# Performance work log

Measured on AMD Instinct MI355X. Metric: run time of the kernel, lower is better.

Reference implementation:

```python
import jax, jax.numpy as jnp
import numpy as np

B, N, DIM, HEADS, DH = 2, 1024, 1024, 16, 64
SEQ_LEN, MEM_NUM = 1024, 4
EH, EW, ET = 4, 4, 1  # mem_expand_size
PH, PW = 4, 4        # patch grid
CUR_PATCH_IDX = 5
MEM_IDXS = [0, 1, 4, 5]


def _locate(idx):
    # get_pos_from_idx_down_right
    num_frame = PH * PW
    inner = idx % num_frame
    return (inner % PH, inner // PH, idx // num_frame)


def _rel_idxs():
    rph, rpw = 2 * EH + 1, 2 * EW + 1
    frame = rph * rpw
    src = _locate(CUR_PATCH_IDX)
    out = []
    for t in MEM_IDXS + [CUR_PATCH_IDX]:
        tg = _locate(t)
        out.append((tg[0] - src[0] + EH) * rpw + (tg[1] - src[1] + EW) + (tg[2] - src[2] + ET) * frame)
    return np.array(out, np.int32)


def setup_inputs() -> dict:
    key = jax.random.key(0)
    ks = jax.random.split(key, 8)
    inner = HEADS * DH
    s = 0.02
    return {
        "x": jax.random.normal(ks[0], (B, N, DIM), jnp.float32),
        "mem": jax.random.normal(ks[1], (B, MEM_NUM * SEQ_LEN, DIM), jnp.float32),
        "mask": jnp.zeros((B, MEM_NUM * SEQ_LEN + N), bool),
        "rel_idxs": jnp.asarray(_rel_idxs()),
        "Wq": jax.random.normal(ks[2], (DIM, inner), jnp.float32) * s,
        "Wk": jax.random.normal(ks[3], (DIM, inner), jnp.float32) * s,
        "Wv": jax.random.normal(ks[4], (DIM, inner), jnp.float32) * s,
        "Wo": jax.random.normal(ks[5], (inner, DIM), jnp.float32) * s,
        "bo": jnp.zeros((DIM,), jnp.float32),
        "rel_table": jax.random.normal(ks[6], ((2 * EH + 1) * (2 * EW + 1) * (2 * ET + 1), HEADS), jnp.float32) * s,
    }


def reference(x, mem, mask, rel_idxs, Wq, Wk, Wv, Wo, bo, rel_table):
    b, n, dim = x.shape
    heads = rel_table.shape[1]
    dh = Wq.shape[1] // heads
    mem_num = rel_idxs.shape[0] - 1
    mem_len = mem.shape[1]
    seq_len = mem_len // mem_num
    scale = dh ** (-0.5)

    kx = jnp.concatenate([mem, x], axis=1)           # [b, j, dim]
    j = kx.shape[1]
    q = (x @ Wq).reshape(b, n, heads, dh).transpose(0, 2, 1, 3)   # bhid
    k = (kx @ Wk).reshape(b, j, heads, dh).transpose(0, 2, 1, 3)  # bhjd
    v = (kx @ Wv).reshape(b, j, heads, dh).transpose(0, 2, 1, 3)

    # relative position bias: a per-head scalar added to every K feature
    rel_emb = rel_table[rel_idxs].T                  # [h, mem_num+1]
    bias_mem = jnp.repeat(rel_emb[:, :mem_num], seq_len, axis=1)  # [h, mem_len]
    bias_cur = jnp.broadcast_to(rel_emb[:, -1:], (heads, j - mem_len))
    bias = jnp.concatenate([bias_mem, bias_cur], axis=1)          # [h, j]
    k = k + bias[None, :, :, None]

    dots = jnp.einsum('bhid,bhjd->bhij', q, k) * scale
    neg = -jnp.finfo(dots.dtype).max
    dots = jnp.where(mask[:, None, None, :], neg, dots)
    causal = jnp.triu(jnp.ones((n, j), bool), j - n + 1)
    dots = jnp.where(causal, neg, dots)

    attn = jax.nn.softmax(dots, axis=-1)
    out = jnp.einsum('bhij,bhjd->bhid', attn, v)
    out = out.transpose(0, 2, 1, 3).reshape(b, n, heads * dh) @ Wo + bo
    new_mem = x[:, -seq_len:]
    return out, new_mem
```

## Files before the change

kernel.cpp:

```cpp
#include <hip/hip_runtime.h>
#include <float.h>

#define NQ    1024
#define JTOT  5120
#define MEML  4096
#define SCL2  0.18033688011112042f

typedef __attribute__((ext_vector_type(8))) short bf16x8;
typedef __attribute__((ext_vector_type(8))) unsigned short ush8;
typedef __attribute__((ext_vector_type(4))) unsigned short ush4;
typedef __attribute__((ext_vector_type(4))) float f32x4;

static __device__ __forceinline__ unsigned short f2bf(float x) {
    union { float f; unsigned u; } v; v.f = x;
    unsigned r = (v.u + 0x7fffu + ((v.u >> 16) & 1u)) >> 16;
    return (unsigned short)r;
}
static __device__ __forceinline__ unsigned pack2(float f0, float f1) {
    union { float f; unsigned u; } a, b; a.f = f1; b.f = f0;
    return __builtin_amdgcn_perm(a.u, b.u, 0x07060302u);
}

static __device__ __forceinline__ void gld16(const void* g, void* l) {
    __builtin_amdgcn_global_load_lds(
        (const __attribute__((address_space(1))) unsigned int*)g,
        (__attribute__((address_space(3))) unsigned int*)l, 16, 0, 0);
}

__global__ __launch_bounds__(256)
void prep_kernel(const float* __restrict__ x, const float* __restrict__ mem,
                 const unsigned char* __restrict__ mask,
                 const float* __restrict__ W0, const float* __restrict__ W1,
                 const float* __restrict__ W2, const float* __restrict__ W3,
                 unsigned short* __restrict__ xb, unsigned short* __restrict__ memb,
                 unsigned short* __restrict__ wt, float* __restrict__ mbp)
{
    __shared__ float Ts[32][33];
    const int bid = blockIdx.x;
    const int t   = threadIdx.x;
    if (bid < 5120) {
        const float* src = (bid < 1024) ? x : mem;
        unsigned short* dst = (bid < 1024) ? xb : memb;
        const size_t i = (size_t)((bid < 1024) ? bid : bid - 1024) * 2048 + t * 8;
        float4 a = *(const float4*)(src + i);
        float4 b = *(const float4*)(src + i + 4);
        ush8 o;
        o[0] = f2bf(a.x); o[1] = f2bf(a.y); o[2] = f2bf(a.z); o[3] = f2bf(a.w);
        o[4] = f2bf(b.x); o[5] = f2bf(b.y); o[6] = f2bf(b.z); o[7] = f2bf(b.w);
        *(ush8*)(dst + i) = o;
    } else if (bid < 5160) {
        const int i = (bid - 5120) * 256 + t;
        mbp[i] = mask[i] ? -1.0e30f : 0.0f;
    } else {
        const int idx = bid - 5160;
        const int z   = idx >> 10;
        const int rem = idx & 1023;
        const float* W = (z == 0) ? W0 : (z == 1) ? W1 : (z == 2) ? W2 : W3;
        unsigned short* D = wt + (size_t)z * 1024 * 1024;
        const int n0 = (rem & 31) * 32, k0 = (rem >> 5) * 32;
        const int tr = t >> 3, tc = (t & 7) * 4;
        float4 v = *(const float4*)(W + (size_t)(k0 + tr) * 1024 + n0 + tc);
        Ts[tr][tc + 0] = v.x; Ts[tr][tc + 1] = v.y;
        Ts[tr][tc + 2] = v.z; Ts[tr][tc + 3] = v.w;
        __syncthreads();
        ush4 o;
        o[0] = f2bf(Ts[tc + 0][tr]); o[1] = f2bf(Ts[tc + 1][tr]);
        o[2] = f2bf(Ts[tc + 2][tr]); o[3] = f2bf(Ts[tc + 3][tr]);
        *(ush4*)(D + (size_t)(n0 + tr) * 1024 + k0 + tc) = o;
    }
}

__global__ __launch_bounds__(256)
void mgemm01_kernel(const unsigned short* __restrict__ xb,
                    const unsigned short* __restrict__ memb,
                    const unsigned short* __restrict__ wt,
                    unsigned short* __restrict__ Qb, unsigned short* __restrict__ Kb,
                    unsigned short* __restrict__ Vb,
                    const float* __restrict__ rel_table, const int* __restrict__ rel_idxs)
{
    __shared__ unsigned short Al[128 * 64];
    __shared__ unsigned short Bl[128 * 64];

    const int t    = threadIdx.x;
    const int lane = t & 63;
    const int w    = t >> 6;
    const int wr   = w >> 1, wc = w & 1;
    const int l15  = lane & 15;
    const int quad = lane >> 4;
    const int l7   = l15 & 7;

    int bid = blockIdx.x;
    int mode, bx, by;
    if (bid < 384) { mode = 0; bx = bid % 24; by = bid / 24; }
    else           { mode = 1; bid -= 384; bx = bid & 15; by = bid >> 4; }
    const int mat = bx >> 3;
    const int n0  = (bx & 7) * 128;
    const int m0  = by * 128;
    const unsigned short* A = (mode == 0) ? xb : memb;
    const unsigned short* B = wt + (size_t)((mode == 0) ? mat : mat + 1) * 1024 * 1024;

    f32x4 acc[4][4];
    #pragma unroll
    for (int i = 0; i < 4; i++)
        #pragma unroll
        for (int j = 0; j < 4; j++) acc[i][j] = (f32x4){0.f, 0.f, 0.f, 0.f};

    for (int k0 = 0; k0 < 1024; k0 += 64) {
        __syncthreads();
        #pragma unroll
        for (int it = 0; it < 4; it++) {
            const int lin  = it * 256 + t;
            const int row  = lin >> 3;
            const int colb = ((lin & 7) ^ (row & 7)) * 8;
            unsigned short* albase = &Al[(size_t)(it * 256 + w * 64) * 8];
            unsigned short* blbase = &Bl[(size_t)(it * 256 + w * 64) * 8];
            gld16(A + (size_t)(m0 + row) * 1024 + k0 + colb, albase);
            gld16(B + (size_t)(n0 + row) * 1024 + k0 + colb, blbase);
        }
        __syncthreads();
        bf16x8 af[4][2], bfr[4][2];
        #pragma unroll
        for (int i = 0; i < 4; i++) {
            const int R = wr * 64 + i * 16 + l15;
            af[i][0] = *(const bf16x8*)&Al[R * 64 + ((quad ^ l7) << 3)];
            af[i][1] = *(const bf16x8*)&Al[R * 64 + (((4 | quad) ^ l7) << 3)];
        }
        #pragma unroll
        for (int j = 0; j < 4; j++) {
            const int R = wc * 64 + j * 16 + l15;
            bfr[j][0] = *(const bf16x8*)&Bl[R * 64 + ((quad ^ l7) << 3)];
            bfr[j][1] = *(const bf16x8*)&Bl[R * 64 + (((4 | quad) ^ l7) << 3)];
        }
        #pragma unroll
        for (int i = 0; i < 4; i++)
            #pragma unroll
            for (int j = 0; j < 4; j++) {
                acc[i][j] = __builtin_amdgcn_mfma_f32_16x16x32_bf16(af[i][0], bfr[j][0], acc[i][j], 0, 0, 0);
                acc[i][j] = __builtin_amdgcn_mfma_f32_16x16x32_bf16(af[i][1], bfr[j][1], acc[i][j], 0, 0, 0);
            }
    }

    const bool isQ = (mode == 0) && (mat == 0);
    const bool isK = (mode == 0) ? (mat == 1) : (mat == 0);
    if (!isQ && !isK) {
        #pragma unroll
        for (int i = 0; i < 4; i++) {
            const int r0 = m0 + wr * 64 + i * 16 + quad * 4;
            const int bb = (mode == 0) ? (r0 >> 10) : (r0 >> 12);
            const int j0 = (mode == 0) ? 4096 + (r0 & 1023) : (r0 & 4095);
            #pragma unroll
            for (int jb = 0; jb < 4; jb++) {
                const int col = n0 + wc * 64 + jb * 16 + l15;
                ush4 o;
                o[0] = f2bf(acc[i][jb][0]); o[1] = f2bf(acc[i][jb][1]);
                o[2] = f2bf(acc[i][jb][2]); o[3] = f2bf(acc[i][jb][3]);
                *(ush4*)(Vb + ((size_t)((bb * 16 + (col >> 6)) * 64 + (col & 63))) * JTOT + j0) = o;
            }
        }
    } else {
        #pragma unroll
        for (int i = 0; i < 4; i++)
            #pragma unroll
            for (int reg = 0; reg < 4; reg++) {
                const int r = m0 + wr * 64 + i * 16 + quad * 4 + reg;
                int bb, idx, chunk;
                if (mode == 0) { bb = r >> 10; idx = isK ? 4096 + (r & 1023) : (r & 1023); chunk = 4; }
                else           { bb = r >> 12; idx = r & 4095; chunk = idx >> 10; }
                #pragma unroll
                for (int jb = 0; jb < 4; jb++) {
                    const int col = n0 + wc * 64 + jb * 16 + l15;
                    const int hh = col >> 6, dh = col & 63;
                    float v = acc[i][jb][reg];
                    if (isK) {
                        v += rel_table[rel_idxs[chunk] * 16 + hh];
                        Kb[((size_t)(bb * 16 + hh) * JTOT + idx) * 64 + dh] = f2bf(v);
                    } else {
                        Qb[((size_t)(bb * 16 + hh) * NQ + idx) * 64 + dh] = f2bf(v);
                    }
                }
            }
    }
}

__global__ __launch_bounds__(256)
void mgemm2_kernel(const unsigned short* __restrict__ A,
                   const unsigned short* __restrict__ WT,
                   float* __restrict__ outF, const float* __restrict__ bo,
                   const float* __restrict__ x, float* __restrict__ newmem)
{
    __shared__ unsigned short Al[64 * 64];
    __shared__ unsigned short Bl[128 * 64];

    const int t = threadIdx.x;
    if (blockIdx.z == 1) {
        const int blk = blockIdx.y * 8 + blockIdx.x;
        const size_t base = (size_t)blk * 8192 + t * 4;
        #pragma unroll
        for (int i = 0; i < 8; i++)
            *(float4*)(newmem + base + (size_t)i * 1024) =
                *(const float4*)(x + base + (size_t)i * 1024);
        return;
    }

    const int lane = t & 63;
    const int w    = t >> 6;
    const int l15  = lane & 15;
    const int quad = lane >> 4;
    const int l7   = l15 & 7;
    const int n0   = blockIdx.x * 128;
    const int m0   = blockIdx.y * 64;

    f32x4 acc[4][2];
    #pragma unroll
    for (int i = 0; i < 4; i++)
        #pragma unroll
        for (int j = 0; j < 2; j++) acc[i][j] = (f32x4){0.f, 0.f, 0.f, 0.f};

    for (int k0 = 0; k0 < 1024; k0 += 64) {
        __syncthreads();
        #pragma unroll
        for (int it = 0; it < 2; it++) {
            const int lin  = it * 256 + t;
            const int row  = lin >> 3;
            const int colb = ((lin & 7) ^ (row & 7)) * 8;
            gld16(A + (size_t)(m0 + row) * 1024 + k0 + colb,
                  &Al[(size_t)(it * 256 + w * 64) * 8]);
        }
        #pragma unroll
        for (int it = 0; it < 4; it++) {
            const int lin  = it * 256 + t;
            const int row  = lin >> 3;
            const int colb = ((lin & 7) ^ (row & 7)) * 8;
            gld16(WT + (size_t)(n0 + row) * 1024 + k0 + colb,
                  &Bl[(size_t)(it * 256 + w * 64) * 8]);
        }
        __syncthreads();
        bf16x8 af[4][2], bfr[2][2];
        #pragma unroll
        for (int i = 0; i < 4; i++) {
            const int R = i * 16 + l15;
            af[i][0] = *(const bf16x8*)&Al[R * 64 + ((quad ^ l7) << 3)];
            af[i][1] = *(const bf16x8*)&Al[R * 64 + (((4 | quad) ^ l7) << 3)];
        }
        #pragma unroll
        for (int j = 0; j < 2; j++) {
            const int R = w * 32 + j * 16 + l15;
            bfr[j][0] = *(const bf16x8*)&Bl[R * 64 + ((quad ^ l7) << 3)];
            bfr[j][1] = *(const bf16x8*)&Bl[R * 64 + (((4 | quad) ^ l7) << 3)];
        }
        #pragma unroll
        for (int i = 0; i < 4; i++)
            #pragma unroll
            for (int j = 0; j < 2; j++) {
                acc[i][j] = __builtin_amdgcn_mfma_f32_16x16x32_bf16(af[i][0], bfr[j][0], acc[i][j], 0, 0, 0);
                acc[i][j] = __builtin_amdgcn_mfma_f32_16x16x32_bf16(af[i][1], bfr[j][1], acc[i][j], 0, 0, 0);
            }
    }

    #pragma unroll
    for (int i = 0; i < 4; i++)
        #pragma unroll
        for (int reg = 0; reg < 4; reg++) {
            const int r = m0 + i * 16 + quad * 4 + reg;
            #pragma unroll
            for (int j = 0; j < 2; j++) {
                const int col = n0 + w * 32 + j * 16 + l15;
                outF[(size_t)r * 1024 + col] = acc[i][j][reg] + bo[col];
            }
        }
}

__global__ __launch_bounds__(256)
void attn5_kernel(const unsigned short* __restrict__ qh,
                  const unsigned short* __restrict__ kh,
                  const unsigned short* __restrict__ vt,
                  const float* __restrict__ mb,
                  unsigned short* __restrict__ ao)
{
    __shared__ unsigned short Ks[128 * 64];
    __shared__ unsigned short Vs[64 * 128];
    __shared__ unsigned short Ps[64 * 128];

    const int t    = threadIdx.x;
    const int lane = t & 63;
    const int w    = t >> 6;
    const int l15  = lane & 15;
    const int quad = lane >> 4;
    const int l7   = l15 & 7;
    const int qt   = blockIdx.x;
    const int h    = blockIdx.y;
    const int b    = blockIdx.z;
    const int qbase = qt * 64;
    const int qg    = qbase + w * 16 + l15;

    const unsigned short* qrow = qh + (((size_t)(b * 16 + h) * NQ + qg) << 6);
    const bf16x8 bq0 = *(const bf16x8*)(qrow + quad * 8);
    const bf16x8 bq1 = *(const bf16x8*)(qrow + 32 + quad * 8);

    const int krow = t >> 3;
    const int kcol = (t & 7) * 8;
    const int ksw  = ((t & 7) ^ (krow & 7)) * 8;
    const int vrow = t >> 4;
    const int vu   = t & 15;
    const int vcol = vu * 8;
    const int vsw  = ((vu & 8) | ((vu ^ (vrow & 7)) & 7)) * 8;

    const unsigned short* kbase = kh + (((size_t)(b * 16 + h) * JTOT) << 6);
    const unsigned short* vbase = vt + (((size_t)(b * 16 + h)) << 6) * JTOT;
    const float* mbb = mb + b * JTOT;

    f32x4 oa[4];
    #pragma unroll
    for (int mt = 0; mt < 4; mt++) oa[mt] = (f32x4){0.f, 0.f, 0.f, 0.f};
    float l_i = 0.f;

    const int ntp = (qt + 66) >> 1;

    ush8 kst[4], vst[4];
    #pragma unroll
    for (int p = 0; p < 4; p++)
        kst[p] = *(const ush8*)(kbase + ((size_t)(krow + 32 * p) << 6) + kcol);
    #pragma unroll
    for (int p = 0; p < 4; p++)
        vst[p] = *(const ush8*)(vbase + (size_t)(vrow + 16 * p) * JTOT + vcol);

    for (int jt = 0; jt < ntp; jt++) {
        const int jbase = jt * 128;
        __syncthreads();
        #pragma unroll
        for (int p = 0; p < 4; p++)
            *(ush8*)&Ks[(krow + 32 * p) * 64 + ksw] = kst[p];
        #pragma unroll
        for (int p = 0; p < 4; p++)
            *(ush8*)&Vs[(vrow + 16 * p) * 128 + vsw] = vst[p];
        __syncthreads();

        if (jt + 1 < ntp) {
            const int jb2 = jbase + 128;
            #pragma unroll
            for (int p = 0; p < 4; p++)
                kst[p] = *(const ush8*)(kbase + ((size_t)(jb2 + krow + 32 * p) << 6) + kcol);
            #pragma unroll
            for (int p = 0; p < 4; p++)
                vst[p] = *(const ush8*)(vbase + (size_t)(vrow + 16 * p) * JTOT + jb2 + vcol);
        }

        f32x4 sa[8];
        #pragma unroll
        for (int mt2 = 0; mt2 < 8; mt2++) {
            const int ra = (mt2 * 16 + l15) * 64;
            const bf16x8 ak0 = *(const bf16x8*)&Ks[ra + ((quad ^ l7) << 3)];
            const bf16x8 ak1 = *(const bf16x8*)&Ks[ra + (((4 | quad) ^ l7) << 3)];
            f32x4 s = (f32x4){0.f, 0.f, 0.f, 0.f};
            s = __builtin_amdgcn_mfma_f32_16x16x32_bf16(ak0, bq0, s, 0, 0, 0);
            s = __builtin_amdgcn_mfma_f32_16x16x32_bf16(ak1, bq1, s, 0, 0, 0);
            sa[mt2] = s;
        }

        #pragma unroll
        for (int mt2 = 0; mt2 < 8; mt2++) {
            const float4 mv = *(const float4*)(mbb + jbase + mt2 * 16 + quad * 4);
            sa[mt2][0] = sa[mt2][0] * SCL2 + mv.x;
            sa[mt2][1] = sa[mt2][1] * SCL2 + mv.y;
            sa[mt2][2] = sa[mt2][2] * SCL2 + mv.z;
            sa[mt2][3] = sa[mt2][3] * SCL2 + mv.w;
        }
        if (jt == ntp - 1) {
            const int tl = qg + 4096 - jbase;
            #pragma unroll
            for (int mt2 = 0; mt2 < 8; mt2++)
                #pragma unroll
                for (int r = 0; r < 4; r++)
                    if (mt2 * 16 + quad * 4 + r > tl) sa[mt2][r] = -1.0e30f;
        }

        #pragma unroll
        for (int mt2 = 0; mt2 < 8; mt2++)
            #pragma unroll
            for (int r = 0; r < 4; r++) {
                const float pv = __builtin_amdgcn_exp2f(sa[mt2][r]);
                sa[mt2][r] = pv;
                l_i += pv;
            }

        const int prow = (w * 16 + l15) * 128;
        #pragma unroll
        for (int mt2 = 0; mt2 < 8; mt2++) {
            const int u  = 2 * mt2 + (quad >> 1);
            const int up = (u & 8) | ((u ^ l7) & 7);
            uint2 pk;
            pk.x = pack2(sa[mt2][0], sa[mt2][1]);
            pk.y = pack2(sa[mt2][2], sa[mt2][3]);
            *(uint2*)&Ps[prow + up * 8 + (quad & 1) * 4] = pk;
        }

        #pragma unroll
        for (int s = 0; s < 4; s++) {
            const int u  = quad + 4 * s;
            const int up = (u & 8) | ((u ^ l7) & 7);
            const bf16x8 bp = *(const bf16x8*)&Ps[prow + up * 8];
            #pragma unroll
            for (int mt = 0; mt < 4; mt++) {
                const bf16x8 av = *(const bf16x8*)&Vs[(mt * 16 + l15) * 128 + up * 8];
                oa[mt] = __builtin_amdgcn_mfma_f32_16x16x32_bf16(av, bp, oa[mt], 0, 0, 0);
            }
        }
    }

    float l = l_i;
    l += __shfl_xor(l, 16);
    l += __shfl_xor(l, 32);
    const float inv = 1.0f / l;
    unsigned short* arow = ao + ((size_t)(b * NQ + qg)) * 1024 + h * 64;
    #pragma unroll
    for (int mt = 0; mt < 4; mt++) {
        ush4 o;
        o[0] = f2bf(oa[mt][0] * inv); o[1] = f2bf(oa[mt][1] * inv);
        o[2] = f2bf(oa[mt][2] * inv); o[3] = f2bf(oa[mt][3] * inv);
        *(ush4*)(arow + mt * 16 + quad * 4) = o;
    }
}

extern "C" void kernel_launch(void* const* d_in, const int* in_sizes, int n_in,
                              void* d_out, int out_size, void* d_ws, size_t ws_size,
                              hipStream_t stream)
{
    const float* x        = (const float*)d_in[0];
    const float* mem      = (const float*)d_in[1];
    const unsigned char* mask = (const unsigned char*)d_in[2];
    const int*   rel_idxs = (const int*)d_in[3];
    const float* Wq       = (const float*)d_in[4];
    const float* Wk       = (const float*)d_in[5];
    const float* Wv       = (const float*)d_in[6];
    const float* Wo       = (const float*)d_in[7];
    const float* bo       = (const float*)d_in[8];
    const float* rel_table= (const float*)d_in[9];

    float* out = (float*)d_out;
    const size_t M1 = (size_t)1024 * 1024;
    unsigned short* xb   = (unsigned short*)d_ws;
    unsigned short* memb = xb   + 2 * M1;
    unsigned short* wt   = memb + 8 * M1;
    unsigned short* qb   = wt   + 4 * M1;
    unsigned short* kb   = qb   + 2 * M1;
    unsigned short* vb   = kb   + 10 * M1;
    unsigned short* aob  = vb   + 10 * M1;
    float* mbp = (float*)(aob + 2 * M1);

    prep_kernel<<<9256, 256, 0, stream>>>(
        x, mem, mask, Wq, Wk, Wv, Wo, xb, memb, wt, mbp);
    mgemm01_kernel<<<1408, 256, 0, stream>>>(
        xb, memb, wt, qb, kb, vb, rel_table, rel_idxs);
    attn5_kernel<<<dim3(16, 16, 2), 256, 0, stream>>>(qb, kb, vb, mbp, aob);
    mgemm2_kernel<<<dim3(8, 32, 2), 256, 0, stream>>>(
        aob, wt + 3 * M1, out, bo, x, out + (size_t)2048 * 1024);
}
```

Before: 323.4 us.

## Rewrite QKV projection GEMM with 256x256 tiles and double-buffered LDS pipeline

Replaces the 128x128 single-buffered QKV/mem projection GEMM with 256x256 tiles on 512-thread blocks and two LDS buffers. Global-to-LDS loads for the next K steps are interleaved between MFMA phases, with explicit vmcnt waits, barriers and setprio, so memory latency overlaps compute and each tile is reused more. In exchange it uses 128KB of LDS and more accumulator registers per thread, and the grid shrinks to 352 blocks, which may underfill the CUs.

Result: slower. 334.1 us (+3.3%).

```diff
diff --git a/kernel.cpp b/kernel.cpp
--- a/kernel.cpp
+++ b/kernel.cpp
@@ -70,7 +70,7 @@
     }
 }
 
-__global__ __launch_bounds__(256)
+__global__ __launch_bounds__(512, 2)
 void mgemm01_kernel(const unsigned short* __restrict__ xb,
                     const unsigned short* __restrict__ memb,
                     const unsigned short* __restrict__ wt,
@@ -78,99 +78,153 @@
                     unsigned short* __restrict__ Vb,
                     const float* __restrict__ rel_table, const int* __restrict__ rel_idxs)
 {
-    __shared__ unsigned short Al[128 * 64];
-    __shared__ unsigned short Bl[128 * 64];
+    __shared__ unsigned short Al[2][256 * 64];
+    __shared__ unsigned short Bl[2][256 * 64];
 
     const int t    = threadIdx.x;
     const int lane = t & 63;
     const int w    = t >> 6;
-    const int wr   = w >> 1, wc = w & 1;
+    const int wr   = w >> 2;
+    const int wc   = w & 3;
     const int l15  = lane & 15;
     const int quad = lane >> 4;
     const int l7   = l15 & 7;
+    const int srow = lane >> 3;
+    const int scol = ((lane & 7) ^ srow) << 3;
 
     int bid = blockIdx.x;
     int mode, bx, by;
-    if (bid < 384) { mode = 0; bx = bid % 24; by = bid / 24; }
-    else           { mode = 1; bid -= 384; bx = bid & 15; by = bid >> 4; }
-    const int mat = bx >> 3;
-    const int n0  = (bx & 7) * 128;
-    const int m0  = by * 128;
-    const unsigned short* A = (mode == 0) ? xb : memb;
-    const unsigned short* B = wt + (size_t)((mode == 0) ? mat : mat + 1) * 1024 * 1024;
-
-    f32x4 acc[4][4];
-    #pragma unroll
-    for (int i = 0; i < 4; i++)
+    if (bid < 96) { mode = 0; bx = bid % 12; by = bid / 12; }
+    else          { bid -= 96; mode = 1; bx = bid & 7; by = bid >> 3; }
+    const int mat = bx >> 2;
+    const int n0  = (bx & 3) << 8;
+    const int m0  = by << 8;
+    const unsigned short* Ag = (mode == 0) ? xb : memb;
+    const unsigned short* Bg = wt + (size_t)((mode == 0) ? mat : mat + 1) * 1024 * 1024;
+
+    const size_t abase = (size_t)(m0 + srow) * 1024 + scol;
+    const size_t bbase = (size_t)(n0 + srow) * 1024 + scol;
+
+    auto stageB0 = [&](int b, int kt) {
+        const int kb = kt << 6, r0 = w * 16;
+        gld16(Bg + bbase + (size_t)r0 * 1024 + kb,       &Bl[b][r0 * 64]);
+        gld16(Bg + bbase + (size_t)(r0 + 8) * 1024 + kb, &Bl[b][(r0 + 8) * 64]);
+    };
+    auto stageB1 = [&](int b, int kt) {
+        const int kb = kt << 6, r0 = 128 + w * 16;
+        gld16(Bg + bbase + (size_t)r0 * 1024 + kb,       &Bl[b][r0 * 64]);
+        gld16(Bg + bbase + (size_t)(r0 + 8) * 1024 + kb, &Bl[b][(r0 + 8) * 64]);
+    };
+    auto stageA1 = [&](int b, int kt) {
+        const int kb = kt << 6, r0 = w * 8, r1 = 128 + w * 8;
+        gld16(Ag + abase + (size_t)r0 * 1024 + kb, &Al[b][r0 * 64]);
+        gld16(Ag + abase + (size_t)r1 * 1024 + kb, &Al[b][r1 * 64]);
+    };
+    auto stageA2 = [&](int b, int kt) {
+        const int kb = kt << 6, r0 = 64 + w * 8, r1 = 192 + w * 8;
+        gld16(Ag + abase + (size_t)r0 * 1024 + kb, &Al[b][r0 * 64]);
+        gld16(Ag + abase + (size_t)r1 * 1024 + kb, &Al[b][r1 * 64]);
+    };
+
+    f32x4 acc[8][4];
+    #pragma unroll
+    for (int i = 0; i < 8; i++)
         #pragma unroll
         for (int j = 0; j < 4; j++) acc[i][j] = (f32x4){0.f, 0.f, 0.f, 0.f};
 
-    for (int k0 = 0; k0 < 1024; k0 += 64) {
-        __syncthreads();
-        #pragma unroll
-        for (int it = 0; it < 4; it++) {
-            const int lin  = it * 256 + t;
-            const int row  = lin >> 3;
-            const int colb = ((lin & 7) ^ (row & 7)) * 8;
-            unsigned short* albase = &Al[(size_t)(it * 256 + w * 64) * 8];
-            unsigned short* blbase = &Bl[(size_t)(it * 256 + w * 64) * 8];
-            gld16(A + (size_t)(m0 + row) * 1024 + k0 + colb, albase);
-            gld16(B + (size_t)(n0 + row) * 1024 + k0 + colb, blbase);
-        }
-        __syncthreads();
-        bf16x8 af[4][2], bfr[4][2];
-        #pragma unroll
-        for (int i = 0; i < 4; i++) {
-            const int R = wr * 64 + i * 16 + l15;
-            af[i][0] = *(const bf16x8*)&Al[R * 64 + ((quad ^ l7) << 3)];
-            af[i][1] = *(const bf16x8*)&Al[R * 64 + (((4 | quad) ^ l7) << 3)];
-        }
-        #pragma unroll
-        for (int j = 0; j < 4; j++) {
-            const int R = wc * 64 + j * 16 + l15;
-            bfr[j][0] = *(const bf16x8*)&Bl[R * 64 + ((quad ^ l7) << 3)];
-            bfr[j][1] = *(const bf16x8*)&Bl[R * 64 + (((4 | quad) ^ l7) << 3)];
-        }
-        #pragma unroll
-        for (int i = 0; i < 4; i++)
-            #pragma unroll
-            for (int j = 0; j < 4; j++) {
-                acc[i][j] = __builtin_amdgcn_mfma_f32_16x16x32_bf16(af[i][0], bfr[j][0], acc[i][j], 0, 0, 0);
-                acc[i][j] = __builtin_amdgcn_mfma_f32_16x16x32_bf16(af[i][1], bfr[j][1], acc[i][j], 0, 0, 0);
-            }
-    }
+    stageB0(0, 0); stageB1(0, 0); stageA1(0, 0); stageA2(0, 0);
+    stageB0(1, 1); stageA1(1, 1); stageB1(1, 1);
+    asm volatile("s_waitcnt vmcnt(6)" ::: "memory");
+    asm volatile("s_barrier" ::: "memory");
+
+    bf16x8 bfr[4][2];
+
+#define PHASE(P, MB, STAGE, VMW)                                                   \
+    {                                                                              \
+        const int Ra0 = (wr * 128 + (MB) * 16 + l15) * 64;                         \
+        const int Ra1 = Ra0 + 16 * 64;                                             \
+        const bf16x8 a0 = *(const bf16x8*)&Al[P][Ra0 + ((quad ^ l7) << 3)];        \
+        const bf16x8 a1 = *(const bf16x8*)&Al[P][Ra0 + (((4 | quad) ^ l7) << 3)];  \
+        const bf16x8 a2 = *(const bf16x8*)&Al[P][Ra1 + ((quad ^ l7) << 3)];        \
+        const bf16x8 a3 = *(const bf16x8*)&Al[P][Ra1 + (((4 | quad) ^ l7) << 3)];  \
+        STAGE;                                                                     \
+        VMW;                                                                       \
+        asm volatile("s_barrier" ::: "memory");                                    \
+        __builtin_amdgcn_s_setprio(1);                                             \
+        _Pragma("unroll")                                                          \
+        for (int n = 0; n < 4; n++) {                                              \
+            acc[(MB)][n]     = __builtin_amdgcn_mfma_f32_16x16x32_bf16(a0, bfr[n][0], acc[(MB)][n], 0, 0, 0);     \
+            acc[(MB)][n]     = __builtin_amdgcn_mfma_f32_16x16x32_bf16(a1, bfr[n][1], acc[(MB)][n], 0, 0, 0);     \
+            acc[(MB) + 1][n] = __builtin_amdgcn_mfma_f32_16x16x32_bf16(a2, bfr[n][0], acc[(MB) + 1][n], 0, 0, 0); \
+            acc[(MB) + 1][n] = __builtin_amdgcn_mfma_f32_16x16x32_bf16(a3, bfr[n][1], acc[(MB) + 1][n], 0, 0, 0); \
+        }                                                                          \
+        __builtin_amdgcn_s_setprio(0);                                             \
+        asm volatile("s_waitcnt lgkmcnt(0)" ::: "memory");                         \
+        asm volatile("s_barrier" ::: "memory");                                    \
+    }
+
+#define KSTEP(P, S0, S1, S2, S3, VMW)                                              \
+    {                                                                              \
+        _Pragma("unroll")                                                          \
+        for (int n = 0; n < 4; n++) {                                              \
+            const int Rb = (wc * 64 + n * 16 + l15) * 64;                          \
+            bfr[n][0] = *(const bf16x8*)&Bl[P][Rb + ((quad ^ l7) << 3)];           \
+            bfr[n][1] = *(const bf16x8*)&Bl[P][Rb + (((4 | quad) ^ l7) << 3)];     \
+        }                                                                          \
+        PHASE(P, 0, S0, {})                                                        \
+        PHASE(P, 2, S1, {})                                                        \
+        PHASE(P, 4, S2, {})                                                        \
+        PHASE(P, 6, S3, VMW)                                                       \
+    }
+
+    #pragma unroll 2
+    for (int tk = 0; tk < 14; ++tk) {
+        const int p = tk & 1;
+        KSTEP(p,
+              stageA2(p ^ 1, tk + 1),
+              stageB0(p, tk + 2),
+              stageA1(p, tk + 2),
+              stageB1(p, tk + 2),
+              asm volatile("s_waitcnt vmcnt(6)" ::: "memory"));
+    }
+    KSTEP(0, stageA2(1, 15), (void)0, (void)0, (void)0,
+          asm volatile("s_waitcnt vmcnt(0)" ::: "memory"));
+    KSTEP(1, (void)0, (void)0, (void)0, (void)0, (void)0);
+
+#undef KSTEP
+#undef PHASE
 
     const bool isQ = (mode == 0) && (mat == 0);
     const bool isK = (mode == 0) ? (mat == 1) : (mat == 0);
     if (!isQ && !isK) {
         #pragma unroll
-        for (int i = 0; i < 4; i++) {
-            const int r0 = m0 + wr * 64 + i * 16 + quad * 4;
+        for (int m = 0; m < 8; m++) {
+            const int r0 = m0 + wr * 128 + m * 16 + quad * 4;
             const int bb = (mode == 0) ? (r0 >> 10) : (r0 >> 12);
             const int j0 = (mode == 0) ? 4096 + (r0 & 1023) : (r0 & 4095);
             #pragma unroll
-            for (int jb = 0; jb < 4; jb++) {
-                const int col = n0 + wc * 64 + jb * 16 + l15;
+            for (int n = 0; n < 4; n++) {
+                const int col = n0 + wc * 64 + n * 16 + l15;
                 ush4 o;
-                o[0] = f2bf(acc[i][jb][0]); o[1] = f2bf(acc[i][jb][1]);
-                o[2] = f2bf(acc[i][jb][2]); o[3] = f2bf(acc[i][jb][3]);
+                o[0] = f2bf(acc[m][n][0]); o[1] = f2bf(acc[m][n][1]);
+                o[2] = f2bf(acc[m][n][2]); o[3] = f2bf(acc[m][n][3]);
                 *(ush4*)(Vb + ((size_t)((bb * 16 + (col >> 6)) * 64 + (col & 63))) * JTOT + j0) = o;
             }
         }
     } else {
         #pragma unroll
-        for (int i = 0; i < 4; i++)
+        for (int m = 0; m < 8; m++)
             #pragma unroll
             for (int reg = 0; reg < 4; reg++) {
-                const int r = m0 + wr * 64 + i * 16 + quad * 4 + reg;
+                const int r = m0 + wr * 128 + m * 16 + quad * 4 + reg;
                 int bb, idx, chunk;
                 if (mode == 0) { bb = r >> 10; idx = isK ? 4096 + (r & 1023) : (r & 1023); chunk = 4; }
                 else           { bb = r >> 12; idx = r & 4095; chunk = idx >> 10; }
                 #pragma unroll
-                for (int jb = 0; jb < 4; jb++) {
-                    const int col = n0 + wc * 64 + jb * 16 + l15;
+                for (int n = 0; n < 4; n++) {
+                    const int col = n0 + wc * 64 + n * 16 + l15;
                     const int hh = col >> 6, dh = col & 63;
-                    float v = acc[i][jb][reg];
+                    float v = acc[m][n][reg];
                     if (isK) {
                         v += rel_table[rel_idxs[chunk] * 16 + hh];
                         Kb[((size_t)(bb * 16 + hh) * JTOT + idx) * 64 + dh] = f2bf(v);
@@ -449,7 +503,7 @@
 
     prep_kernel<<<9256, 256, 0, stream>>>(
         x, mem, mask, Wq, Wk, Wv, Wo, xb, memb, wt, mbp);
-    mgemm01_kernel<<<1408, 256, 0, stream>>>(
+    mgemm01_kernel<<<352, 512, 0, stream>>>(
         xb, memb, wt, qb, kb, vb, rel_table, rel_idxs);
     attn5_kernel<<<dim3(16, 16, 2), 256, 0, stream>>>(qb, kb, vb, mbp, aob);
     mgemm2_kernel<<<dim3(8, 32, 2), 256, 0, stream>>>(
```

## Split attention QK work across waves by key tile and add XCD-aware block mapping

Applied to the files above, without the earlier changes.

In the attention kernel, each wave now computes scores for all 64 queries against its own 32-key slice, not its 16 queries against all 128 keys. This removes the 4x redundant K-fragment LDS reads per wave, at the cost of an extra barrier before the PV step and a cross-wave row-sum reduction through shared memory. Block indices in both the attention kernel and the QKV GEMM are remapped so blocks sharing a head or weight panel land on the same XCD for L2 reuse. s_setprio hints are also placed around the MFMA sections.

Measured after the change: 292.9 us. 1.1x faster.

```diff
diff --git a/kernel.cpp b/kernel.cpp
--- a/kernel.cpp
+++ b/kernel.cpp
@@ -89,10 +89,20 @@
     const int quad = lane >> 4;
     const int l7   = l15 & 7;
 
-    int bid = blockIdx.x;
+    const int bid = blockIdx.x;
     int mode, bx, by;
-    if (bid < 384) { mode = 0; bx = bid % 24; by = bid / 24; }
-    else           { mode = 1; bid -= 384; bx = bid & 15; by = bid >> 4; }
+    if (bid < 384) {
+        mode = 0;
+        const int c = bid & 7, i = bid >> 3;
+        bx = 3 * c + i % 3;
+        by = i / 3;
+    } else {
+        mode = 1;
+        const int p = bid - 384;
+        const int c = p & 7, i = p >> 3;
+        bx = i & 15;
+        by = 8 * c + (i >> 4);
+    }
     const int mat = bx >> 3;
     const int n0  = (bx & 7) * 128;
     const int m0  = by * 128;
@@ -271,7 +281,7 @@
 }
 
 __global__ __launch_bounds__(256)
-void attn5_kernel(const unsigned short* __restrict__ qh,
+void attn6_kernel(const unsigned short* __restrict__ qh,
                   const unsigned short* __restrict__ kh,
                   const unsigned short* __restrict__ vt,
                   const float* __restrict__ mb,
@@ -280,6 +290,7 @@
     __shared__ unsigned short Ks[128 * 64];
     __shared__ unsigned short Vs[64 * 128];
     __shared__ unsigned short Ps[64 * 128];
+    __shared__ float Ls[4][64];
 
     const int t    = threadIdx.x;
     const int lane = t & 63;
@@ -287,15 +298,26 @@
     const int l15  = lane & 15;
     const int quad = lane >> 4;
     const int l7   = l15 & 7;
-    const int qt   = blockIdx.x;
-    const int h    = blockIdx.y;
-    const int b    = blockIdx.z;
+
+    const int flat = blockIdx.x + 16 * blockIdx.y + 256 * blockIdx.z;
+    const int xcd  = flat & 7;
+    const int idx  = flat >> 3;
+    const int qt   = idx >> 2;
+    const int hb   = (xcd << 2) | (idx & 3);
+    const int h    = hb & 15;
+    const int b    = hb >> 4;
+
     const int qbase = qt * 64;
     const int qg    = qbase + w * 16 + l15;
 
-    const unsigned short* qrow = qh + (((size_t)(b * 16 + h) * NQ + qg) << 6);
-    const bf16x8 bq0 = *(const bf16x8*)(qrow + quad * 8);
-    const bf16x8 bq1 = *(const bf16x8*)(qrow + 32 + quad * 8);
+    bf16x8 bq0[4], bq1[4];
+    #pragma unroll
+    for (int qb = 0; qb < 4; qb++) {
+        const unsigned short* qrow =
+            qh + (((size_t)(b * 16 + h) * NQ + qbase + qb * 16 + l15) << 6);
+        bq0[qb] = *(const bf16x8*)(qrow + quad * 8);
+        bq1[qb] = *(const bf16x8*)(qrow + 32 + quad * 8);
+    }
 
     const int krow = t >> 3;
     const int kcol = (t & 7) * 8;
@@ -312,7 +334,7 @@
     f32x4 oa[4];
     #pragma unroll
     for (int mt = 0; mt < 4; mt++) oa[mt] = (f32x4){0.f, 0.f, 0.f, 0.f};
-    float l_i = 0.f;
+    float lacc[4] = {0.f, 0.f, 0.f, 0.f};
 
     const int ntp = (qt + 66) >> 1;
 
@@ -324,6 +346,8 @@
     for (int p = 0; p < 4; p++)
         vst[p] = *(const ush8*)(vbase + (size_t)(vrow + 16 * p) * JTOT + vcol);
 
+    const int prow = (w * 16 + l15) * 128;
+
     for (int jt = 0; jt < ntp; jt++) {
         const int jbase = jt * 128;
         __syncthreads();
@@ -345,55 +369,73 @@
                 vst[p] = *(const ush8*)(vbase + (size_t)(vrow + 16 * p) * JTOT + jb2 + vcol);
         }
 
-        f32x4 sa[8];
-        #pragma unroll
-        for (int mt2 = 0; mt2 < 8; mt2++) {
-            const int ra = (mt2 * 16 + l15) * 64;
+        f32x4 sa[2][4];
+        __builtin_amdgcn_s_setprio(1);
+        #pragma unroll
+        for (int kk = 0; kk < 2; kk++) {
+            const int mt2 = 2 * w + kk;
+            const int ra  = (mt2 * 16 + l15) * 64;
             const bf16x8 ak0 = *(const bf16x8*)&Ks[ra + ((quad ^ l7) << 3)];
             const bf16x8 ak1 = *(const bf16x8*)&Ks[ra + (((4 | quad) ^ l7) << 3)];
-            f32x4 s = (f32x4){0.f, 0.f, 0.f, 0.f};
-            s = __builtin_amdgcn_mfma_f32_16x16x32_bf16(ak0, bq0, s, 0, 0, 0);
-            s = __builtin_amdgcn_mfma_f32_16x16x32_bf16(ak1, bq1, s, 0, 0, 0);
-            sa[mt2] = s;
-        }
-
-        #pragma unroll
-        for (int mt2 = 0; mt2 < 8; mt2++) {
-            const float4 mv = *(const float4*)(mbb + jbase + mt2 * 16 + quad * 4);
-            sa[mt2][0] = sa[mt2][0] * SCL2 + mv.x;
-            sa[mt2][1] = sa[mt2][1] * SCL2 + mv.y;
-            sa[mt2][2] = sa[mt2][2] * SCL2 + mv.z;
-            sa[mt2][3] = sa[mt2][3] * SCL2 + mv.w;
+            #pragma unroll
+            for (int qb = 0; qb < 4; qb++) {
+                f32x4 s = (f32x4){0.f, 0.f, 0.f, 0.f};
+                s = __builtin_amdgcn_mfma_f32_16x16x32_bf16(ak0, bq0[qb], s, 0, 0, 0);
+                s = __builtin_amdgcn_mfma_f32_16x16x32_bf16(ak1, bq1[qb], s, 0, 0, 0);
+                sa[kk][qb] = s;
+            }
+        }
+        __builtin_amdgcn_s_setprio(0);
+
+        #pragma unroll
+        for (int kk = 0; kk < 2; kk++) {
+            const float4 mv = *(const float4*)(mbb + jbase + (2 * w + kk) * 16 + quad * 4);
+            #pragma unroll
+            for (int qb = 0; qb < 4; qb++) {
+                sa[kk][qb][0] = sa[kk][qb][0] * SCL2 + mv.x;
+                sa[kk][qb][1] = sa[kk][qb][1] * SCL2 + mv.y;
+                sa[kk][qb][2] = sa[kk][qb][2] * SCL2 + mv.z;
+                sa[kk][qb][3] = sa[kk][qb][3] * SCL2 + mv.w;
+            }
         }
         if (jt == ntp - 1) {
-            const int tl = qg + 4096 - jbase;
-            #pragma unroll
-            for (int mt2 = 0; mt2 < 8; mt2++)
+            #pragma unroll
+            for (int qb = 0; qb < 4; qb++) {
+                const int tl = qbase + qb * 16 + l15 + 4096 - jbase;
                 #pragma unroll
-                for (int r = 0; r < 4; r++)
-                    if (mt2 * 16 + quad * 4 + r > tl) sa[mt2][r] = -1.0e30f;
-        }
-
-        #pragma unroll
-        for (int mt2 = 0; mt2 < 8; mt2++)
-            #pragma unroll
-            for (int r = 0; r < 4; r++) {
-                const float pv = __builtin_amdgcn_exp2f(sa[mt2][r]);
-                sa[mt2][r] = pv;
-                l_i += pv;
-            }
-
-        const int prow = (w * 16 + l15) * 128;
-        #pragma unroll
-        for (int mt2 = 0; mt2 < 8; mt2++) {
-            const int u  = 2 * mt2 + (quad >> 1);
+                for (int kk = 0; kk < 2; kk++)
+                    #pragma unroll
+                    for (int r = 0; r < 4; r++)
+                        if ((2 * w + kk) * 16 + quad * 4 + r > tl) sa[kk][qb][r] = -1.0e30f;
+            }
+        }
+
+        #pragma unroll
+        for (int kk = 0; kk < 2; kk++)
+            #pragma unroll
+            for (int qb = 0; qb < 4; qb++)
+                #pragma unroll
+                for (int r = 0; r < 4; r++) {
+                    const float pv = __builtin_amdgcn_exp2f(sa[kk][qb][r]);
+                    sa[kk][qb][r] = pv;
+                    lacc[qb] += pv;
+                }
+
+        #pragma unroll
+        for (int kk = 0; kk < 2; kk++) {
+            const int u  = 4 * w + 2 * kk + (quad >> 1);
             const int up = (u & 8) | ((u ^ l7) & 7);
-            uint2 pk;
-            pk.x = pack2(sa[mt2][0], sa[mt2][1]);
-            pk.y = pack2(sa[mt2][2], sa[mt2][3]);
-            *(uint2*)&Ps[prow + up * 8 + (quad & 1) * 4] = pk;
-        }
-
+            #pragma unroll
+            for (int qb = 0; qb < 4; qb++) {
+                uint2 pk;
+                pk.x = pack2(sa[kk][qb][0], sa[kk][qb][1]);
+                pk.y = pack2(sa[kk][qb][2], sa[kk][qb][3]);
+                *(uint2*)&Ps[(qb * 16 + l15) * 128 + up * 8 + (quad & 1) * 4] = pk;
+            }
+        }
+        __syncthreads();
+
+        __builtin_amdgcn_s_setprio(1);
         #pragma unroll
         for (int s = 0; s < 4; s++) {
             const int u  = quad + 4 * s;
@@ -405,11 +447,21 @@
                 oa[mt] = __builtin_amdgcn_mfma_f32_16x16x32_bf16(av, bp, oa[mt], 0, 0, 0);
             }
         }
-    }
-
-    float l = l_i;
-    l += __shfl_xor(l, 16);
-    l += __shfl_xor(l, 32);
+        __builtin_amdgcn_s_setprio(0);
+    }
+
+    #pragma unroll
+    for (int qb = 0; qb < 4; qb++) {
+        lacc[qb] += __shfl_xor(lacc[qb], 16);
+        lacc[qb] += __shfl_xor(lacc[qb], 32);
+    }
+    if (quad == 0) {
+        #pragma unroll
+        for (int qb = 0; qb < 4; qb++) Ls[w][qb * 16 + l15] = lacc[qb];
+    }
+    __syncthreads();
+    const float l = Ls[0][w * 16 + l15] + Ls[1][w * 16 + l15] +
+                    Ls[2][w * 16 + l15] + Ls[3][w * 16 + l15];
     const float inv = 1.0f / l;
     unsigned short* arow = ao + ((size_t)(b * NQ + qg)) * 1024 + h * 64;
     #pragma unroll
@@ -451,7 +503,7 @@
         x, mem, mask, Wq, Wk, Wv, Wo, xb, memb, wt, mbp);
     mgemm01_kernel<<<1408, 256, 0, stream>>>(
         xb, memb, wt, qb, kb, vb, rel_table, rel_idxs);
-    attn5_kernel<<<dim3(16, 16, 2), 256, 0, stream>>>(qb, kb, vb, mbp, aob);
+    attn6_kernel<<<dim3(16, 16, 2), 256, 0, stream>>>(qb, kb, vb, mbp, aob);
     mgemm2_kernel<<<dim3(8, 32, 2), 256, 0, stream>>>(
         aob, wt + 3 * M1, out, bo, x, out + (size_t)2048 * 1024);
 }
```
